# Kernel optimization log

Measured on AMD Instinct MI355X. Metric: run time of the kernel, lower is better.

## Reference

```python
import jax, jax.numpy as jnp
import numpy as np

IN_FEATURES = 4096
BATCH = 2048
OUT_FEATURES = IN_FEATURES + 2


def setup_inputs() -> dict:
    key = jax.random.key(0)
    k1, k2, k3 = jax.random.split(key, 3)
    stdv = 1.0 / np.sqrt(IN_FEATURES)
    x = jax.random.normal(k1, (BATCH, IN_FEATURES), dtype=jnp.float32)
    weight = jax.random.uniform(k2, (OUT_FEATURES, IN_FEATURES), minval=-stdv, maxval=stdv, dtype=jnp.float32)
    bias = jax.random.uniform(k3, (OUT_FEATURES,), minval=-stdv, maxval=stdv, dtype=jnp.float32)
    return {"x": x, "weight": weight, "bias": bias}


def _spread_forward(x, weight, bias):
    # Faithful to the torch loop: for each n, only weight[n:n+3, n] contributes
    # (band width 3), added to output cols [n, n+3); then the *running* output
    # window [n, n+3) is multiplied by (1 + bias[n:n+3]). The bias step makes
    # this a sequential recurrence over n -> lax.scan.
    B, n_in = x.shape
    n_out = n_in + 2
    idx = jnp.arange(n_in)
    off = jnp.arange(3)
    # w_band[n, k] = weight[n + k, n]   (the only weights the mask keeps)
    w_band = weight[idx[:, None] + off[None, :], idx[:, None]]  # [n_in, 3]
    b_win = bias[idx[:, None] + off[None, :]]                   # [n_in, 3]
    x_cols = x.T                                                # [n_in, B]

    def step(out, scan_in):
        n, wb, bw, xn = scan_in
        window = jax.lax.dynamic_slice(out, (0, n), (B, 3))     # [B, 3]
        window = (window + xn[:, None] * wb[None, :]) * (1.0 + bw[None, :])
        out = jax.lax.dynamic_update_slice(out, window, (0, n))
        return out, None

    out0 = jnp.zeros((B, n_out), dtype=x.dtype)
    out, _ = jax.lax.scan(step, out0, (idx, w_band, b_win, x_cols))
    return out


def reference(x, weight, bias):
    return _spread_forward(x, weight, bias)
```

## Files before the change

kernel.cpp:

```cpp
#include <hip/hip_runtime.h>


constexpr int N_IN  = 4096;
constexpr int N_OUT = 4098;
constexpr int BATCH = 2048;
constexpr int ROWS  = 4;

__global__ __launch_bounds__(256) void coeff_kernel(
    const float* __restrict__ weight, const float* __restrict__ bias,
    float* __restrict__ c) {
  int m = blockIdx.x * blockDim.x + threadIdx.x;
  if (m >= N_OUT) return;
  float s  = 1.0f + bias[m];
  float s2 = s * s;
  float s3 = s2 * s;
  int red = (m > N_IN - 1) ? (m - (N_IN - 1)) : 0;
#pragma unroll
  for (int j = 0; j < 3; ++j) {
    int n = m - j;
    float cj = 0.0f;
    if (n >= 0 && n < N_IN) {
      int pw = j + 1 - red;
      float sp = (pw == 1) ? s : ((pw == 2) ? s2 : s3);
      cj = weight[(size_t)m * N_IN + n] * sp;
    }
    c[j * N_OUT + m] = cj;
  }
}

__global__ __launch_bounds__(256) void spread_kernel(
    const float* __restrict__ x, const float* __restrict__ c,
    float* __restrict__ out) {
  int pair = blockIdx.x * blockDim.x + threadIdx.x;
  if (pair >= N_OUT / 2) return;
  int m0 = pair * 2;

  float c00 = c[m0],             c01 = c[m0 + 1];
  float c10 = c[N_OUT + m0],     c11 = c[N_OUT + m0 + 1];
  float c20 = c[2 * N_OUT + m0], c21 = c[2 * N_OUT + m0 + 1];

  int lo_i = (m0 >= 2) ? (m0 - 2) : 0;
  int hi_i = (m0 <= N_IN - 2) ? m0 : (N_IN - 2);

  int b0 = blockIdx.y * ROWS;
#pragma unroll
  for (int r = 0; r < ROWS; ++r) {
    int b = b0 + r;
    const float* xrow = x + (size_t)b * N_IN;
    float2 lo = *(const float2*)(xrow + lo_i);
    float2 hi = *(const float2*)(xrow + hi_i);
    float o0 = c00 * hi.x + c10 * lo.y + c20 * lo.x;
    float o1 = c01 * hi.y + c11 * hi.x + c21 * lo.y;
    *(float2*)(out + (size_t)b * N_OUT + m0) = make_float2(o0, o1);
  }
}

extern "C" void kernel_launch(void* const* d_in, const int* in_sizes, int n_in,
                              void* d_out, int out_size, void* d_ws, size_t ws_size,
                              hipStream_t stream) {
  const float* x    = (const float*)d_in[0];
  const float* w    = (const float*)d_in[1];
  const float* bias = (const float*)d_in[2];
  float* out = (float*)d_out;
  float* c   = (float*)d_ws;

  coeff_kernel<<<dim3((N_OUT + 255) / 256), dim3(256), 0, stream>>>(w, bias, c);

  dim3 grid((N_OUT / 2 + 255) / 256, BATCH / ROWS);
  spread_kernel<<<grid, dim3(256), 0, stream>>>(x, c, out);
}
```

Baseline: 124.5 us.

## Fuse coefficient computation into spread kernel with nontemporal stores and more rows

Removes the separate coefficient kernel and has each thread compute its banded weight-times-bias-power coefficients inline, eliminating one launch and the workspace round trip. Rows per block grow from 4 to 16 so the per-thread coefficient gathers (strided weight reads) are amortized over more batch rows. Output stores become nontemporal to reduce cache pollution on the large streaming write. The trade-off is redundant coefficient gathers across the batch-row grid and fewer, larger blocks.

```diff
diff --git a/kernel.cpp b/kernel.cpp
--- a/kernel.cpp
+++ b/kernel.cpp
@@ -4,40 +4,41 @@
 constexpr int N_IN  = 4096;
 constexpr int N_OUT = 4098;
 constexpr int BATCH = 2048;
-constexpr int ROWS  = 4;
+constexpr int ROWS  = 16;
 
-__global__ __launch_bounds__(256) void coeff_kernel(
-    const float* __restrict__ weight, const float* __restrict__ bias,
-    float* __restrict__ c) {
-  int m = blockIdx.x * blockDim.x + threadIdx.x;
-  if (m >= N_OUT) return;
-  float s  = 1.0f + bias[m];
-  float s2 = s * s;
-  float s3 = s2 * s;
-  int red = (m > N_IN - 1) ? (m - (N_IN - 1)) : 0;
-#pragma unroll
-  for (int j = 0; j < 3; ++j) {
-    int n = m - j;
-    float cj = 0.0f;
-    if (n >= 0 && n < N_IN) {
-      int pw = j + 1 - red;
-      float sp = (pw == 1) ? s : ((pw == 2) ? s2 : s3);
-      cj = weight[(size_t)m * N_IN + n] * sp;
-    }
-    c[j * N_OUT + m] = cj;
-  }
-}
+typedef float v2f __attribute__((ext_vector_type(2)));
 
-__global__ __launch_bounds__(256) void spread_kernel(
-    const float* __restrict__ x, const float* __restrict__ c,
-    float* __restrict__ out) {
+__global__ __launch_bounds__(256) void spread_fused(
+    const float* __restrict__ x, const float* __restrict__ weight,
+    const float* __restrict__ bias, float* __restrict__ out) {
   int pair = blockIdx.x * blockDim.x + threadIdx.x;
   if (pair >= N_OUT / 2) return;
   int m0 = pair * 2;
 
-  float c00 = c[m0],             c01 = c[m0 + 1];
-  float c10 = c[N_OUT + m0],     c11 = c[N_OUT + m0 + 1];
-  float c20 = c[2 * N_OUT + m0], c21 = c[2 * N_OUT + m0 + 1];
+  float c00, c10, c20, c01, c11, c21;
+  {
+    float ctmp[2][3];
+#pragma unroll
+    for (int k = 0; k < 2; ++k) {
+      int m = m0 + k;
+      float s  = 1.0f + bias[m];
+      float s2 = s * s;
+      int red = (m > N_IN - 1) ? (m - (N_IN - 1)) : 0;
+#pragma unroll
+      for (int j = 0; j < 3; ++j) {
+        int n = m - j;
+        float cj = 0.0f;
+        if (n >= 0 && n < N_IN) {
+          int p = j + 1 - red;
+          float sp = (p == 1) ? s : ((p == 2) ? s2 : s2 * s);
+          cj = weight[(size_t)m * N_IN + n] * sp;
+        }
+        ctmp[k][j] = cj;
+      }
+    }
+    c00 = ctmp[0][0]; c10 = ctmp[0][1]; c20 = ctmp[0][2];
+    c01 = ctmp[1][0]; c11 = ctmp[1][1]; c21 = ctmp[1][2];
+  }
 
   int lo_i = (m0 >= 2) ? (m0 - 2) : 0;
   int hi_i = (m0 <= N_IN - 2) ? m0 : (N_IN - 2);
@@ -47,11 +48,13 @@
   for (int r = 0; r < ROWS; ++r) {
     int b = b0 + r;
     const float* xrow = x + (size_t)b * N_IN;
-    float2 lo = *(const float2*)(xrow + lo_i);
-    float2 hi = *(const float2*)(xrow + hi_i);
+    v2f lo = *(const v2f*)(xrow + lo_i);
+    v2f hi = *(const v2f*)(xrow + hi_i);
     float o0 = c00 * hi.x + c10 * lo.y + c20 * lo.x;
     float o1 = c01 * hi.y + c11 * hi.x + c21 * lo.y;
-    *(float2*)(out + (size_t)b * N_OUT + m0) = make_float2(o0, o1);
+    v2f res; res.x = o0; res.y = o1;
+    v2f* dst = (v2f*)(out + (size_t)b * N_OUT + m0);
+    __builtin_nontemporal_store(res, dst);
   }
 }
 
@@ -62,10 +65,7 @@
   const float* w    = (const float*)d_in[1];
   const float* bias = (const float*)d_in[2];
   float* out = (float*)d_out;
-  float* c   = (float*)d_ws;
-
-  coeff_kernel<<<dim3((N_OUT + 255) / 256), dim3(256), 0, stream>>>(w, bias, c);
 
   dim3 grid((N_OUT / 2 + 255) / 256, BATCH / ROWS);
-  spread_kernel<<<grid, dim3(256), 0, stream>>>(x, c, out);
+  spread_fused<<<grid, dim3(256), 0, stream>>>(x, w, bias, out);
 }
```

Result: slower. 127.1 us (+2.1%).
